# Performance work log

Hardware: AMD Instinct MI355X
Metric: run time of the kernel (lower is better)

Reference implementation:

```python
import jax, jax.numpy as jnp
import numpy as np

DIM = 256
HEAD_DIM = 64
NH = DIM // HEAD_DIM
PS = 2  # fine patch size
EPS = 1e-5


def _conv(x, w, b, stride, pad):
    y = jax.lax.conv_general_dilated(x, w, (stride, stride), ((pad, pad), (pad, pad)),
                                     dimension_numbers=('NCHW', 'OIHW', 'NCHW'))
    return y + b[None, :, None, None]


def _bn(x, g, b, m, v):
    s = g * jax.lax.rsqrt(v + EPS)
    return x * s[None, :, None, None] + (b - m * s)[None, :, None, None]


def setup_inputs() -> dict:
    key = jax.random.key(0)
    ks = jax.random.split(key, 24)
    C = DIM
    d = {}
    d['x'] = jax.random.normal(ks[0], (8, C, 64, 64), jnp.float32)
    # Downsample conv (C->C, k=4, s=2, p=1), torch OIHW layout
    d['w_down'] = jax.random.normal(ks[1], (C, C, 4, 4), jnp.float32) * 0.02
    d['b_down'] = jax.random.normal(ks[2], (C,), jnp.float32) * 0.02
    # coarse to_qkv Linear(64 -> 192), stored as [in, out]
    d['w_qkv_c'] = jax.random.normal(ks[3], (HEAD_DIM, 3 * HEAD_DIM), jnp.float32) * 0.05
    d['b_qkv_c'] = jax.random.normal(ks[4], (3 * HEAD_DIM,), jnp.float32) * 0.02
    # Upsample ConvTranspose2d (torch [in, out, kH, kW] layout)
    d['w_up'] = jax.random.normal(ks[5], (C, C, 4, 4), jnp.float32) * 0.02
    d['b_up'] = jax.random.normal(ks[6], (C,), jnp.float32) * 0.02
    # fine to_qkv Linear(64 -> 192)
    d['w_qkv_f'] = jax.random.normal(ks[7], (HEAD_DIM, 3 * HEAD_DIM), jnp.float32) * 0.05
    d['b_qkv_f'] = jax.random.normal(ks[8], (3 * HEAD_DIM,), jnp.float32) * 0.02
    # DWConv: depthwise 3x3 (groups=C) -> BN -> relu6 -> pointwise 1x1 -> BN -> relu6
    d['w_dw'] = jax.random.normal(ks[9], (C, 1, 3, 3), jnp.float32) * 0.1
    d['bn_dw_g'] = jax.random.uniform(ks[10], (C,), jnp.float32) * 0.5 + 0.75
    d['bn_dw_b'] = jax.random.normal(ks[11], (C,), jnp.float32) * 0.1
    d['bn_dw_m'] = jax.random.normal(ks[12], (C,), jnp.float32) * 0.1
    d['bn_dw_v'] = jax.random.uniform(ks[13], (C,), jnp.float32) + 0.5
    d['w_pw'] = jax.random.normal(ks[14], (C, C, 1, 1), jnp.float32) * 0.05
    d['bn_pw_g'] = jax.random.uniform(ks[15], (C,), jnp.float32) * 0.5 + 0.75
    d['bn_pw_b'] = jax.random.normal(ks[16], (C,), jnp.float32) * 0.1
    d['bn_pw_m'] = jax.random.normal(ks[17], (C,), jnp.float32) * 0.1
    d['bn_pw_v'] = jax.random.uniform(ks[18], (C,), jnp.float32) + 0.5
    return d


def reference(x, w_down, b_down, w_qkv_c, b_qkv_c, w_up, b_up, w_qkv_f, b_qkv_f,
              w_dw, bn_dw_g, bn_dw_b, bn_dw_m, bn_dw_v,
              w_pw, bn_pw_g, bn_pw_b, bn_pw_m, bn_pw_v):
    B, C, H, W = x.shape
    nh, hd = C // HEAD_DIM, HEAD_DIM
    scale = hd ** -0.5

    # ---- CoarseSelfAttention ----
    xd = _conv(x, w_down, b_down, 2, 1)           # [B,C,h,w]
    h, w = xd.shape[2], xd.shape[3]
    P = h * w
    tok = xd.reshape(B, nh, hd, P).transpose(0, 1, 3, 2)   # [B,nh,P,hd]
    q, k, v = jnp.split(tok @ w_qkv_c + b_qkv_c, 3, axis=-1)
    attn = jax.nn.softmax(jnp.einsum('bhqd,bhkd->bhqk', q, k) * scale, axis=-1)
    coarse_score = attn.sum(axis=-2)               # [B,nh,P]
    kf = max(1, P // 4)
    top_k = jax.lax.top_k(coarse_score, kf)[1]     # [B,nh,kf]
    out = jnp.einsum('bhqk,bhkd->bhqd', attn, v)
    out = out.transpose(0, 1, 3, 2).reshape(B, C, h, w)
    # ConvTranspose2d(k=4,s=2,p=1) as lhs-dilated conv with flipped/transposed kernel
    wt = jnp.flip(w_up, (2, 3)).transpose(1, 0, 2, 3)
    coarse = jax.lax.conv_general_dilated(out, wt, (1, 1), ((2, 2), (2, 2)),
                                          lhs_dilation=(2, 2),
                                          dimension_numbers=('NCHW', 'OIHW', 'NCHW'))
    coarse = coarse + b_up[None, :, None, None]
    # F.interpolate to (H,W) is identity here: upsample exactly restores HxW

    # ---- TopkSelfAttention ----
    ph, pw = H // PS, W // PS                      # ph*pw == P
    xh = coarse.reshape(B, nh, hd, ph, PS, pw, PS)
    patches = xh.transpose(0, 1, 2, 3, 5, 4, 6).reshape(B, nh, hd, ph * pw, PS, PS)
    idx = jnp.broadcast_to(top_k[:, :, None, :, None, None], (B, nh, hd, kf, PS, PS))
    sel = jnp.take_along_axis(patches, idx, axis=3)        # [B,nh,hd,kf,PS,PS]
    tokf = sel.reshape(B, nh, hd, kf, PS * PS).transpose(0, 1, 3, 4, 2)
    tokf = tokf.reshape(B, nh, kf * PS * PS, hd)
    qf, kk, vf = jnp.split(tokf @ w_qkv_f + b_qkv_f, 3, axis=-1)
    attnf = jax.nn.softmax(jnp.einsum('bhqd,bhkd->bhqk', qf, kk) * scale, axis=-1)
    outf = jnp.einsum('bhqk,bhkd->bhqd', attnf, vf)
    outf = outf.reshape(B, nh, kf, PS * PS, hd).transpose(0, 1, 2, 4, 3)
    outf = outf.reshape(B, nh, kf, hd, PS, PS)     # [B,nh,kf,hd,PS,PS]
    # scatter selected patches back into zeros (topk indices are unique per b,h)
    res = jnp.zeros((B, nh, ph * pw, hd, PS, PS), x.dtype)
    bi = jnp.arange(B)[:, None, None]
    hi = jnp.arange(nh)[None, :, None]
    res = res.at[bi, hi, top_k].set(outf)
    res = res.transpose(0, 1, 3, 2, 4, 5).reshape(B, nh, hd, ph, pw, PS, PS)
    region = res.transpose(0, 1, 2, 3, 5, 4, 6).reshape(B, C, H, W)

    y = coarse + region

    # ---- DWConv feed-forward ----
    yd = jax.lax.conv_general_dilated(y, w_dw, (1, 1), ((1, 1), (1, 1)),
                                      feature_group_count=C,
                                      dimension_numbers=('NCHW', 'OIHW', 'NCHW'))
    yd = jnp.clip(_bn(yd, bn_dw_g, bn_dw_b, bn_dw_m, bn_dw_v), 0.0, 6.0)
    yp = jax.lax.conv_general_dilated(yd, w_pw, (1, 1), ((0, 0), (0, 0)),
                                      dimension_numbers=('NCHW', 'OIHW', 'NCHW'))
    yp = jnp.clip(_bn(yp, bn_pw_g, bn_pw_b, bn_pw_m, bn_pw_v), 0.0, 6.0)
    return yp
```

## Files before the change

kernel.cpp:

```cpp
#include <hip/hip_runtime.h>
#include <cstdint>
#include <cstddef>


#define EPS_ 1e-5f

typedef short bf16x8_t __attribute__((ext_vector_type(8)));
typedef float f32x4_t __attribute__((ext_vector_type(4)));
#define MFMA16(a, b, c) __builtin_amdgcn_mfma_f32_16x16x32_bf16(a, b, c, 0, 0, 0)

__device__ __forceinline__ void cvt1(float f, unsigned short& h, unsigned short& l) {
  unsigned u = __float_as_uint(f);
  unsigned r = u + 0x7FFFu + ((u >> 16) & 1u);
  h = (unsigned short)(r >> 16);
  float lo = f - __uint_as_float(r & 0xFFFF0000u);
  l = (unsigned short)(__float_as_uint(lo) >> 16);
}
__device__ __forceinline__ unsigned cvtpack(float f) {
  unsigned short h, l;
  cvt1(f, h, l);
  return (unsigned)h | ((unsigned)l << 16);
}
__device__ __forceinline__ void cvt2(float f0, float f1, unsigned& hpack, unsigned& lpack) {
  unsigned u0 = __float_as_uint(f0), u1 = __float_as_uint(f1);
  unsigned r0 = u0 + 0x7FFFu + ((u0 >> 16) & 1u);
  unsigned r1 = u1 + 0x7FFFu + ((u1 >> 16) & 1u);
  hpack = (r0 >> 16) | (r1 & 0xFFFF0000u);
  float l0 = f0 - __uint_as_float(r0 & 0xFFFF0000u);
  float l1 = f1 - __uint_as_float(r1 & 0xFFFF0000u);
  lpack = (__float_as_uint(l0) >> 16) | (__float_as_uint(l1) & 0xFFFF0000u);
}
__device__ __forceinline__ unsigned pk_h(unsigned a, unsigned b) {
  return (a & 0xFFFFu) | (b << 16);
}
__device__ __forceinline__ unsigned pk_l(unsigned a, unsigned b) {
  return (a >> 16) | (b & 0xFFFF0000u);
}

__global__ __launch_bounds__(256) void k_pad_x(
    const float* __restrict__ x, unsigned* __restrict__ xphl) {
  const int plane = blockIdx.x;
  const float* src = x + (size_t)plane * 4096;
  unsigned* dst = xphl + (size_t)plane * 4488;
  for (int e = threadIdx.x; e < 4356; e += 256) {
    int r = e / 66, cc = e - r * 66;
    float v = 0.f;
    if (r >= 1 && r <= 64 && cc >= 1 && cc <= 64) v = src[(r - 1) * 64 + (cc - 1)];
    dst[r * 68 + cc] = cvtpack(v);
  }
}

__global__ __launch_bounds__(256) void k_cvt_wdown(
    const float* __restrict__ w, unsigned short* __restrict__ wh,
    unsigned short* __restrict__ wl) {
  int e = blockIdx.x * 256 + threadIdx.x;
  cvt1(w[e], wh[e], wl[e]);
}

__global__ __launch_bounds__(256) void k_cvt_wqkv(
    const float* __restrict__ wq, unsigned short* __restrict__ wh,
    unsigned short* __restrict__ wl) {
  int e = blockIdx.x * 256 + threadIdx.x;
  int col = e >> 6, d = e & 63;
  float f = wq[d * 192 + col];
  if (col < 64) f *= 0.125f;
  cvt1(f, wh[e], wl[e]);
}

__global__ __launch_bounds__(256) void k_cvt_wup(
    const float* __restrict__ w_up, unsigned short* __restrict__ wth,
    unsigned short* __restrict__ wtl) {
  int e = blockIdx.x * 256 + threadIdx.x;
  int kp = e & 1023, oc = (e >> 10) & 255, c = e >> 18;
  int tap = kp >> 8, ic = kp & 255;
  int tk = tap >> 1, txi = tap & 1;
  int ry = c >> 1, rx = c & 1;
  int ky = (1 - ry) + 2 * tk, kx = (1 - rx) + 2 * txi;
  cvt1(w_up[((size_t)(ic * 256 + oc) * 4 + ky) * 4 + kx], wth[e], wtl[e]);
}

__global__ __launch_bounds__(256) void k_cvt_wpw(
    const float* __restrict__ w, unsigned short* __restrict__ wh,
    unsigned short* __restrict__ wl) {
  int e = blockIdx.x * 256 + threadIdx.x;
  cvt1(w[e], wh[e], wl[e]);
}

__device__ __forceinline__ void mfma_chunk(
    const unsigned short (*Ah)[72], const unsigned short (*Al)[72],
    const unsigned short (*Bh)[72], const unsigned short (*Bl)[72],
    f32x4_t (&acc)[4], int wm, int lane) {
  const int l16 = lane & 15, quad = lane >> 4;
#pragma unroll
  for (int ks = 0; ks < 2; ++ks) {
    int ko = ks * 32 + quad * 8;
    bf16x8_t ah = *(const bf16x8_t*)&Ah[wm + l16][ko];
    bf16x8_t al = *(const bf16x8_t*)&Al[wm + l16][ko];
#pragma unroll
    for (int nt = 0; nt < 4; ++nt) {
      bf16x8_t bh = *(const bf16x8_t*)&Bh[nt * 16 + l16][ko];
      bf16x8_t bl = *(const bf16x8_t*)&Bl[nt * 16 + l16][ko];
      acc[nt] = MFMA16(ah, bh, acc[nt]);
      acc[nt] = MFMA16(ah, bl, acc[nt]);
      acc[nt] = MFMA16(al, bh, acc[nt]);
    }
  }
}

__device__ __forceinline__ void mfma_tile2x2(
    const unsigned short (*Ah)[72], const unsigned short (*Al)[72],
    const unsigned short (*Bh)[72], const unsigned short (*Bl)[72],
    f32x4_t (&acc)[2][2], int wm, int wn, int lane) {
  const int l16 = lane & 15, quad = lane >> 4;
#pragma unroll
  for (int ks = 0; ks < 2; ++ks) {
    int ko = ks * 32 + quad * 8;
    bf16x8_t ah[2], al[2];
#pragma unroll
    for (int mt = 0; mt < 2; ++mt) {
      ah[mt] = *(const bf16x8_t*)&Ah[wm + mt * 16 + l16][ko];
      al[mt] = *(const bf16x8_t*)&Al[wm + mt * 16 + l16][ko];
    }
#pragma unroll
    for (int nt = 0; nt < 2; ++nt) {
      bf16x8_t bh = *(const bf16x8_t*)&Bh[wn + nt * 16 + l16][ko];
      bf16x8_t bl = *(const bf16x8_t*)&Bl[wn + nt * 16 + l16][ko];
#pragma unroll
      for (int mt = 0; mt < 2; ++mt) {
        acc[mt][nt] = MFMA16(ah[mt], bh, acc[mt][nt]);
        acc[mt][nt] = MFMA16(ah[mt], bl, acc[mt][nt]);
        acc[mt][nt] = MFMA16(al[mt], bh, acc[mt][nt]);
      }
    }
  }
}

__device__ __forceinline__ void mfma_tile2x4(
    const unsigned short (*Ah)[72], const unsigned short (*Al)[72],
    const unsigned short (*Bh)[72], const unsigned short (*Bl)[72],
    f32x4_t (&acc)[2][4], int wm, int wn, int lane) {
  const int l16 = lane & 15, quad = lane >> 4;
#pragma unroll
  for (int ks = 0; ks < 2; ++ks) {
    int ko = ks * 32 + quad * 8;
    bf16x8_t ah[2], al[2];
#pragma unroll
    for (int mt = 0; mt < 2; ++mt) {
      ah[mt] = *(const bf16x8_t*)&Ah[wm + mt * 16 + l16][ko];
      al[mt] = *(const bf16x8_t*)&Al[wm + mt * 16 + l16][ko];
    }
#pragma unroll
    for (int nt = 0; nt < 4; ++nt) {
      bf16x8_t bh = *(const bf16x8_t*)&Bh[wn + nt * 16 + l16][ko];
      bf16x8_t bl = *(const bf16x8_t*)&Bl[wn + nt * 16 + l16][ko];
#pragma unroll
      for (int mt = 0; mt < 2; ++mt) {
        acc[mt][nt] = MFMA16(ah[mt], bh, acc[mt][nt]);
        acc[mt][nt] = MFMA16(ah[mt], bl, acc[mt][nt]);
        acc[mt][nt] = MFMA16(al[mt], bh, acc[mt][nt]);
      }
    }
  }
}

__global__ __launch_bounds__(256) void k_conv_down_mfma(
    const unsigned* __restrict__ xphl, const unsigned short* __restrict__ wdh,
    const unsigned short* __restrict__ wdl, const float* __restrict__ bias,
    unsigned* __restrict__ xdhl) {
  __shared__ unsigned short Ah[64][72], Al[64][72], Bh[64][72], Bl[64][72];
  const int t = threadIdx.x;
  const int pix0 = blockIdx.x * 64, oc0 = blockIdx.y * 64;
  const int bimg = pix0 >> 10, pos = pix0 & 1023;
  const int pl = t & 63, icg = t >> 6;
  const int rem = (pix0 + pl) & 1023;
  const int oy = rem >> 5, ox = rem & 31;
  const unsigned* xb = xphl + ((size_t)bimg * 256 + icg) * 4488 + (oy * 2) * 68 + ox * 2;
  const int wave = t >> 6, lane = t & 63, l16 = lane & 15, quad = lane >> 4;
  const int wm = (wave & 1) * 32, wn = (wave >> 1) * 32;
  const int ar = t >> 2, ac = (t & 3) * 16;
  const unsigned short* wra = wdh + (size_t)(oc0 + ar) * 4096 + ac;
  const unsigned short* wrl = wdl + (size_t)(oc0 + ar) * 4096 + ac;
  f32x4_t acc[2][2] = {};
  for (int kb = 0; kb < 4096; kb += 64) {
    bf16x8_t a0 = *(const bf16x8_t*)(wra + kb);
    bf16x8_t a1 = *(const bf16x8_t*)(wra + kb + 8);
    bf16x8_t a2 = *(const bf16x8_t*)(wrl + kb);
    bf16x8_t a3 = *(const bf16x8_t*)(wrl + kb + 8);
    unsigned u[16];
#pragma unroll
    for (int r = 0; r < 4; ++r) {
      uint2 u01 = *(const uint2*)(xb + r * 68);
      uint2 u23 = *(const uint2*)(xb + r * 68 + 2);
      u[4 * r + 0] = u01.x; u[4 * r + 1] = u01.y;
      u[4 * r + 2] = u23.x; u[4 * r + 3] = u23.y;
    }
    unsigned hp[8], lp[8];
#pragma unroll
    for (int j = 0; j < 8; ++j) {
      hp[j] = pk_h(u[2 * j], u[2 * j + 1]);
      lp[j] = pk_l(u[2 * j], u[2 * j + 1]);
    }
    __syncthreads();
    *(bf16x8_t*)&Ah[ar][ac] = a0;
    *(bf16x8_t*)&Ah[ar][ac + 8] = a1;
    *(bf16x8_t*)&Al[ar][ac] = a2;
    *(bf16x8_t*)&Al[ar][ac + 8] = a3;
    *(uint4*)&Bh[pl][icg * 16] = make_uint4(hp[0], hp[1], hp[2], hp[3]);
    *(uint4*)&Bh[pl][icg * 16 + 8] = make_uint4(hp[4], hp[5], hp[6], hp[7]);
    *(uint4*)&Bl[pl][icg * 16] = make_uint4(lp[0], lp[1], lp[2], lp[3]);
    *(uint4*)&Bl[pl][icg * 16 + 8] = make_uint4(lp[4], lp[5], lp[6], lp[7]);
    __syncthreads();
    mfma_tile2x2(Ah, Al, Bh, Bl, acc, wm, wn, lane);
    xb += 4 * 4488;
  }
#pragma unroll
  for (int mt = 0; mt < 2; ++mt)
#pragma unroll
    for (int r = 0; r < 4; ++r) {
      int oc = oc0 + wm + mt * 16 + quad * 4 + r;
      float bv = bias[oc];
#pragma unroll
      for (int nt = 0; nt < 2; ++nt)
        xdhl[((size_t)(bimg * 256 + oc)) * 1024 + pos + wn + nt * 16 + l16] =
            cvtpack(acc[mt][nt][r] + bv);
    }
}

template <int MODE>
__global__ __launch_bounds__(256) void k_qkv_mfma(
    const unsigned* __restrict__ srcp, const float* __restrict__ srcf,
    const unsigned short* __restrict__ wh, const unsigned short* __restrict__ wl,
    const float* __restrict__ bq, const int* __restrict__ topk,
    unsigned short* __restrict__ qh, unsigned short* __restrict__ ql,
    unsigned short* __restrict__ kh, unsigned short* __restrict__ kl,
    unsigned short* __restrict__ vth, unsigned short* __restrict__ vtl) {
  __shared__ unsigned short Ah[64][72], Al[64][72];
  const int t = threadIdx.x;
  const int tok0 = blockIdx.x * 64;
  const int pair = blockIdx.y;
  const int b = pair >> 2, h = pair & 3;
  const int tokl = t & 63, dg = t >> 6;
  unsigned hp[8], lp[8];
  if (MODE == 0) {
    const unsigned* base = srcp + ((size_t)(b * 256 + h * 64 + dg * 16)) * 1024 + tok0 + tokl;
    unsigned u[16];
#pragma unroll
    for (int j = 0; j < 16; ++j) u[j] = base[(size_t)j * 1024];
#pragma unroll
    for (int j = 0; j < 8; ++j) {
      hp[j] = pk_h(u[2 * j], u[2 * j + 1]);
      lp[j] = pk_l(u[2 * j], u[2 * j + 1]);
    }
  } else {
    int tok = tok0 + tokl;
    int pp = topk[pair * 256 + (tok >> 2)];
    int py = (tok >> 1) & 1, px = tok & 1;
    int ry = (pp >> 5) * 2 + py, rx = (pp & 31) * 2 + px;
    const float* base = srcf + ((size_t)(b * 256 + h * 64 + dg * 16)) * 4096 + ry * 64 + rx;
    float fv[16];
#pragma unroll
    for (int j = 0; j < 16; ++j) fv[j] = base[(size_t)j * 4096];
#pragma unroll
    for (int j = 0; j < 8; ++j) cvt2(fv[2 * j], fv[2 * j + 1], hp[j], lp[j]);
  }
  *(uint4*)&Ah[tokl][dg * 16] = make_uint4(hp[0], hp[1], hp[2], hp[3]);
  *(uint4*)&Ah[tokl][dg * 16 + 8] = make_uint4(hp[4], hp[5], hp[6], hp[7]);
  *(uint4*)&Al[tokl][dg * 16] = make_uint4(lp[0], lp[1], lp[2], lp[3]);
  *(uint4*)&Al[tokl][dg * 16 + 8] = make_uint4(lp[4], lp[5], lp[6], lp[7]);
  __syncthreads();
  const int wave = t >> 6, lane = t & 63, l16 = lane & 15, quad = lane >> 4;
  f32x4_t acc[4][3] = {};
#pragma unroll
  for (int ks = 0; ks < 2; ++ks) {
    int ko = ks * 32 + quad * 8;
    bf16x8_t bh0[3], bl0[3];
#pragma unroll
    for (int nt = 0; nt < 3; ++nt) {
      int col = wave * 48 + nt * 16 + l16;
      bh0[nt] = *(const bf16x8_t*)(wh + col * 64 + ko);
      bl0[nt] = *(const bf16x8_t*)(wl + col * 64 + ko);
    }
#pragma unroll
    for (int mt = 0; mt < 4; ++mt) {
      bf16x8_t ah = *(const bf16x8_t*)&Ah[mt * 16 + l16][ko];
      bf16x8_t al = *(const bf16x8_t*)&Al[mt * 16 + l16][ko];
#pragma unroll
      for (int nt = 0; nt < 3; ++nt) {
        acc[mt][nt] = MFMA16(ah, bh0[nt], acc[mt][nt]);
        acc[mt][nt] = MFMA16(ah, bl0[nt], acc[mt][nt]);
        acc[mt][nt] = MFMA16(al, bh0[nt], acc[mt][nt]);
      }
    }
  }
#pragma unroll
  for (int nt = 0; nt < 3; ++nt) {
    int col = wave * 48 + nt * 16 + l16;
    float bqv = bq[col];
    if (col < 64) bqv *= 0.125f;
#pragma unroll
    for (int mt = 0; mt < 4; ++mt) {
#pragma unroll
      for (int r = 0; r < 4; ++r) {
        int tok = tok0 + mt * 16 + quad * 4 + r;
        float val = acc[mt][nt][r] + bqv;
        unsigned short hh, ll;
        cvt1(val, hh, ll);
        if (col < 64) {
          size_t o = ((size_t)pair * 1024 + tok) * 64 + col;
          qh[o] = hh; ql[o] = ll;
        } else if (col < 128) {
          size_t o = ((size_t)pair * 1024 + tok) * 64 + (col - 64);
          kh[o] = hh; kl[o] = ll;
        } else {
          size_t o = ((size_t)pair * 64 + (col - 128)) * 1024 + tok;
          vth[o] = hh; vtl[o] = ll;
        }
      }
    }
  }
}

__global__ __launch_bounds__(256) void k_attn_coarse(
    const unsigned short* __restrict__ qh, const unsigned short* __restrict__ ql,
    const unsigned short* __restrict__ kh, const unsigned short* __restrict__ kl,
    const unsigned short* __restrict__ vth, const unsigned short* __restrict__ vtl,
    float* __restrict__ score, unsigned* __restrict__ outc) {
  __shared__ __align__(16) unsigned short Qb[2][64][72];
  __shared__ __align__(16) unsigned short Kb[2][64][72];
  __shared__ __align__(16) unsigned short Vb[2][64][72];
  __shared__ __align__(16) unsigned short Pb[2][64][72];
  __shared__ float mlW[4][2][64];
  __shared__ float mC[64], lC[64];
  __shared__ float colsum[1024];
  const int t = threadIdx.x;
  const int q0 = blockIdx.x * 64;
  const int pair = blockIdx.y;
  const int wave = t >> 6, lane = t & 63;
  const int l16 = lane & 15, quad = lane >> 4;
  const int wm = wave * 16;
  const int sr = t >> 3, skc = (t & 7) * 8;

  const size_t qbase = ((size_t)pair * 1024 + q0) * 64;
#pragma unroll
  for (int i = 0; i < 2; ++i) {
    int r = sr + i * 32;
    *(bf16x8_t*)&Qb[0][r][skc] = *(const bf16x8_t*)(qh + qbase + (size_t)r * 64 + skc);
    *(bf16x8_t*)&Qb[1][r][skc] = *(const bf16x8_t*)(ql + qbase + (size_t)r * 64 + skc);
  }
#pragma unroll
  for (int i = 0; i < 4; ++i) colsum[t + i * 256] = 0.f;

  const size_t kmbase = (size_t)pair * 1024 * 64;
  const size_t vbase = (size_t)pair * 64 * 1024;

  float mrun[4] = {-1e30f, -1e30f, -1e30f, -1e30f};
  float lrun[4] = {0.f, 0.f, 0.f, 0.f};
  for (int kb = 0; kb < 1024; kb += 64) {
    __syncthreads();
#pragma unroll
    for (int i = 0; i < 2; ++i) {
      int r = sr + i * 32;
      *(bf16x8_t*)&Kb[0][r][skc] = *(const bf16x8_t*)(kh + kmbase + (size_t)(kb + r) * 64 + skc);
      *(bf16x8_t*)&Kb[1][r][skc] = *(const bf16x8_t*)(kl + kmbase + (size_t)(kb + r) * 64 + skc);
    }
    __syncthreads();
    f32x4_t acc[4] = {};
    mfma_chunk(Kb[0], Kb[1], Qb[0], Qb[1], acc, wm, lane);
#pragma unroll
    for (int nt = 0; nt < 4; ++nt) {
      float m0 = fmaxf(fmaxf(acc[nt][0], acc[nt][1]), fmaxf(acc[nt][2], acc[nt][3]));
      m0 = fmaxf(m0, __shfl_xor(m0, 16));
      m0 = fmaxf(m0, __shfl_xor(m0, 32));
      float mn = fmaxf(mrun[nt], m0);
      float s0 = __expf(acc[nt][0] - mn) + __expf(acc[nt][1] - mn) +
                 __expf(acc[nt][2] - mn) + __expf(acc[nt][3] - mn);
      s0 += __shfl_xor(s0, 16);
      s0 += __shfl_xor(s0, 32);
      lrun[nt] = lrun[nt] * __expf(mrun[nt] - mn) + s0;
      mrun[nt] = mn;
    }
  }
  __syncthreads();
  if (quad == 0) {
#pragma unroll
    for (int nt = 0; nt < 4; ++nt) {
      mlW[wave][0][nt * 16 + l16] = mrun[nt];
      mlW[wave][1][nt * 16 + l16] = lrun[nt];
    }
  }
  __syncthreads();
  if (t < 64) {
    float m0 = mlW[0][0][t], m1 = mlW[1][0][t], m2 = mlW[2][0][t], m3 = mlW[3][0][t];
    float mm = fmaxf(fmaxf(m0, m1), fmaxf(m2, m3));
    float ll = mlW[0][1][t] * __expf(m0 - mm) + mlW[1][1][t] * __expf(m1 - mm) +
               mlW[2][1][t] * __expf(m2 - mm) + mlW[3][1][t] * __expf(m3 - mm);
    mC[t] = mm;
    lC[t] = 1.0f / ll;
  }
  __syncthreads();
  float mq[4], il[4];
#pragma unroll
  for (int nt = 0; nt < 4; ++nt) {
    mq[nt] = mC[nt * 16 + l16];
    il[nt] = lC[nt * 16 + l16];
  }

  f32x4_t accO[4] = {};
  for (int kb = 0; kb < 1024; kb += 64) {
    __syncthreads();
#pragma unroll
    for (int i = 0; i < 2; ++i) {
      int r = sr + i * 32;
      *(bf16x8_t*)&Kb[0][r][skc] = *(const bf16x8_t*)(kh + kmbase + (size_t)(kb + r) * 64 + skc);
      *(bf16x8_t*)&Kb[1][r][skc] = *(const bf16x8_t*)(kl + kmbase + (size_t)(kb + r) * 64 + skc);
      *(bf16x8_t*)&Vb[0][r][skc] = *(const bf16x8_t*)(vth + vbase + (size_t)r * 1024 + kb + skc);
      *(bf16x8_t*)&Vb[1][r][skc] = *(const bf16x8_t*)(vtl + vbase + (size_t)r * 1024 + kb + skc);
    }
    __syncthreads();
    f32x4_t acc[4] = {};
    mfma_chunk(Kb[0], Kb[1], Qb[0], Qb[1], acc, wm, lane);
    float P[4][4];
#pragma unroll
    for (int nt = 0; nt < 4; ++nt)
#pragma unroll
      for (int r = 0; r < 4; ++r) P[nt][r] = __expf(acc[nt][r] - mq[nt]) * il[nt];
#pragma unroll
    for (int r = 0; r < 4; ++r) {
      float cs = P[0][r] + P[1][r] + P[2][r] + P[3][r];
      cs += __shfl_xor(cs, 1);
      cs += __shfl_xor(cs, 2);
      cs += __shfl_xor(cs, 4);
      cs += __shfl_xor(cs, 8);
      if (l16 == 0) colsum[kb + wm + quad * 4 + r] += cs;
    }
#pragma unroll
    for (int nt = 0; nt < 4; ++nt) {
      unsigned h01, l01, h23, l23;
      cvt2(P[nt][0], P[nt][1], h01, l01);
      cvt2(P[nt][2], P[nt][3], h23, l23);
      *(uint2*)&Pb[0][nt * 16 + l16][wm + quad * 4] = make_uint2(h01, h23);
      *(uint2*)&Pb[1][nt * 16 + l16][wm + quad * 4] = make_uint2(l01, l23);
    }
    __syncthreads();
    mfma_chunk(Pb[0], Pb[1], Vb[0], Vb[1], accO, wm, lane);
  }
  __syncthreads();

#pragma unroll
  for (int i = 0; i < 4; ++i)
    atomicAdd(&score[pair * 1024 + t + i * 256], colsum[t + i * 256]);
  float (*Tr)[68] = reinterpret_cast<float(*)[68]>(&Pb[0][0][0]);
#pragma unroll
  for (int nt = 0; nt < 4; ++nt)
#pragma unroll
    for (int r = 0; r < 4; ++r)
      Tr[nt * 16 + l16][wm + quad * 4 + r] = accO[nt][r];
  __syncthreads();
  const int b = pair >> 2, h = pair & 3;
#pragma unroll
  for (int i = 0; i < 16; ++i) {
    int e = t + i * 256;
    int d = e >> 6, ql_ = e & 63;
    int pix = q0 + ql_;
    int iy = (pix >> 5) + 1, ix = (pix & 31) + 1;
    outc[((size_t)(b * 256 + h * 64 + d)) * 1156 + iy * 34 + ix] = cvtpack(Tr[d][ql_]);
  }
}

__global__ __launch_bounds__(256) void k_attn_fine(
    const unsigned short* __restrict__ qh, const unsigned short* __restrict__ ql,
    const unsigned short* __restrict__ kh, const unsigned short* __restrict__ kl,
    const unsigned short* __restrict__ vth, const unsigned short* __restrict__ vtl,
    float* __restrict__ outf) {
  __shared__ __align__(16) unsigned short Qb[2][64][72];
  __shared__ __align__(16) unsigned short Kb[2][64][72];
  __shared__ __align__(16) unsigned short Vb[2][64][72];
  __shared__ __align__(16) unsigned short Pb[2][64][72];
  __shared__ float m_run[64], l_run[64], alphaS[64];
  __shared__ float mWc[4][64], sWc[4][64];
  const int t = threadIdx.x;
  const int q0 = blockIdx.x * 64;
  const int pair = blockIdx.y;
  const int wave = t >> 6, lane = t & 63;
  const int l16 = lane & 15, quad = lane >> 4;
  const int wm = wave * 16;
  const int sr = t >> 3, skc = (t & 7) * 8;

  const size_t qbase = ((size_t)pair * 1024 + q0) * 64;
#pragma unroll
  for (int i = 0; i < 2; ++i) {
    int r = sr + i * 32;
    *(bf16x8_t*)&Qb[0][r][skc] = *(const bf16x8_t*)(qh + qbase + (size_t)r * 64 + skc);
    *(bf16x8_t*)&Qb[1][r][skc] = *(const bf16x8_t*)(ql + qbase + (size_t)r * 64 + skc);
  }
  if (t < 64) { m_run[t] = -1e30f; l_run[t] = 0.f; }

  const size_t kmbase = (size_t)pair * 1024 * 64;
  const size_t vbase = (size_t)pair * 64 * 1024;

  f32x4_t accO[4] = {};
  for (int kb = 0; kb < 1024; kb += 64) {
    __syncthreads();
#pragma unroll
    for (int i = 0; i < 2; ++i) {
      int r = sr + i * 32;
      *(bf16x8_t*)&Kb[0][r][skc] = *(const bf16x8_t*)(kh + kmbase + (size_t)(kb + r) * 64 + skc);
      *(bf16x8_t*)&Kb[1][r][skc] = *(const bf16x8_t*)(kl + kmbase + (size_t)(kb + r) * 64 + skc);
      *(bf16x8_t*)&Vb[0][r][skc] = *(const bf16x8_t*)(vth + vbase + (size_t)r * 1024 + kb + skc);
      *(bf16x8_t*)&Vb[1][r][skc] = *(const bf16x8_t*)(vtl + vbase + (size_t)r * 1024 + kb + skc);
    }
    __syncthreads();
    f32x4_t acc[4] = {};
    mfma_chunk(Kb[0], Kb[1], Qb[0], Qb[1], acc, wm, lane);
#pragma unroll
    for (int nt = 0; nt < 4; ++nt) {
      float m0 = fmaxf(fmaxf(acc[nt][0], acc[nt][1]), fmaxf(acc[nt][2], acc[nt][3]));
      m0 = fmaxf(m0, __shfl_xor(m0, 16));
      m0 = fmaxf(m0, __shfl_xor(m0, 32));
      if (quad == 0) mWc[wave][nt * 16 + l16] = m0;
    }
    __syncthreads();
    if (t < 64) {
      float mn = fmaxf(fmaxf(fmaxf(mWc[0][t], mWc[1][t]), fmaxf(mWc[2][t], mWc[3][t])),
                       m_run[t]);
      alphaS[t] = __expf(m_run[t] - mn);
      m_run[t] = mn;
    }
    __syncthreads();
    float P[4][4];
#pragma unroll
    for (int nt = 0; nt < 4; ++nt) {
      float mn = m_run[nt * 16 + l16];
#pragma unroll
      for (int r = 0; r < 4; ++r) P[nt][r] = __expf(acc[nt][r] - mn);
      float s0 = P[nt][0] + P[nt][1] + P[nt][2] + P[nt][3];
      s0 += __shfl_xor(s0, 16);
      s0 += __shfl_xor(s0, 32);
      if (quad == 0) sWc[wave][nt * 16 + l16] = s0;
      unsigned h01, l01, h23, l23;
      cvt2(P[nt][0], P[nt][1], h01, l01);
      cvt2(P[nt][2], P[nt][3], h23, l23);
      *(uint2*)&Pb[0][nt * 16 + l16][wm + quad * 4] = make_uint2(h01, h23);
      *(uint2*)&Pb[1][nt * 16 + l16][wm + quad * 4] = make_uint2(l01, l23);
    }
#pragma unroll
    for (int r = 0; r < 4; ++r) {
      float a = alphaS[wm + quad * 4 + r];
#pragma unroll
      for (int nt = 0; nt < 4; ++nt) accO[nt][r] *= a;
    }
    __syncthreads();
    if (t < 64)
      l_run[t] = l_run[t] * alphaS[t] + (sWc[0][t] + sWc[1][t] + sWc[2][t] + sWc[3][t]);
    mfma_chunk(Pb[0], Pb[1], Vb[0], Vb[1], accO, wm, lane);
  }
  __syncthreads();
#pragma unroll
  for (int r = 0; r < 4; ++r) {
    float invl = 1.0f / l_run[wm + quad * 4 + r];
    int qm = q0 + wm + quad * 4 + r;
#pragma unroll
    for (int nt = 0; nt < 4; ++nt)
      outf[((size_t)pair * 1024 + qm) * 64 + nt * 16 + l16] = accO[nt][r] * invl;
  }
}

__global__ __launch_bounds__(256) void k_topk(
    const float* __restrict__ score, int* __restrict__ idx) {
  __shared__ unsigned long long key[1024];
  const int pair = blockIdx.x;
  const int t = threadIdx.x;
#pragma unroll
  for (int j = 0; j < 4; ++j) {
    int i = t + j * 256;
    unsigned u = __float_as_uint(score[pair * 1024 + i]);
    u = u ^ ((u & 0x80000000u) ? 0xFFFFFFFFu : 0x80000000u);
    u = ~u;
    key[i] = ((unsigned long long)u << 32) | (unsigned)i;
  }
  __syncthreads();
  for (int k = 2; k <= 1024; k <<= 1) {
    for (int j = k >> 1; j > 0; j >>= 1) {
      for (int w = 0; w < 4; ++w) {
        int i = t + w * 256;
        int l = i ^ j;
        if (l > i) {
          bool up = ((i & k) == 0);
          unsigned long long a = key[i], b = key[l];
          if ((a > b) == up) { key[i] = b; key[l] = a; }
        }
      }
      __syncthreads();
    }
  }
  idx[pair * 256 + t] = (int)(key[t] & 0xFFFFFFFFu);
}

__global__ __launch_bounds__(256) void k_convT_mfma(
    const unsigned* __restrict__ inp, const unsigned short* __restrict__ wth,
    const unsigned short* __restrict__ wtl, const float* __restrict__ bias,
    float* __restrict__ out) {
  __shared__ unsigned short Ah[64][72], Al[64][72];
  __shared__ unsigned short Bh[128][72], Bl[128][72];
  const int t = threadIdx.x;
  const int pix0 = blockIdx.x * 128;
  const int oc0 = blockIdx.y * 64;
  const int cls = blockIdx.z;
  const int ry = cls >> 1, rx = cls & 1;
  const int b = pix0 >> 10;
  const int wave = t >> 6, lane = t & 63;
  const int l16 = lane & 15, quad = lane >> 4;
  const int wm = (wave & 1) * 32, wn = (wave >> 1) * 64;
  const int pl = t & 127, icg = t >> 7;
  const int remg = (pix0 + pl) & 1023;
  const int tyy = remg >> 5, txx = remg & 31;
  const int ar = t >> 2, ac = (t & 3) * 16;
  const size_t wbase = ((size_t)cls * 256 + oc0 + ar) * 1024 + ac;
  f32x4_t acc[2][4] = {};
  for (int kb = 0; kb < 1024; kb += 64) {
    const int tap = kb >> 8, ic0 = kb & 255;
    const int tk = tap >> 1, txi = tap & 1;
    const int iy = tyy + ry + 1 - tk, ix = txx + rx + 1 - txi;
    const unsigned* p = inp + (size_t)(b * 256 + ic0 + icg * 32) * 1156 + iy * 34 + ix;
    unsigned u[32];
#pragma unroll
    for (int j = 0; j < 32; ++j) u[j] = p[(size_t)j * 1156];
    unsigned hp[16], lpk[16];
#pragma unroll
    for (int j = 0; j < 16; ++j) {
      hp[j] = pk_h(u[2 * j], u[2 * j + 1]);
      lpk[j] = pk_l(u[2 * j], u[2 * j + 1]);
    }
    bf16x8_t a0 = *(const bf16x8_t*)(wth + wbase + kb);
    bf16x8_t a1 = *(const bf16x8_t*)(wth + wbase + kb + 8);
    bf16x8_t a2 = *(const bf16x8_t*)(wtl + wbase + kb);
    bf16x8_t a3 = *(const bf16x8_t*)(wtl + wbase + kb + 8);
    __syncthreads();
    *(bf16x8_t*)&Ah[ar][ac] = a0;
    *(bf16x8_t*)&Ah[ar][ac + 8] = a1;
    *(bf16x8_t*)&Al[ar][ac] = a2;
    *(bf16x8_t*)&Al[ar][ac + 8] = a3;
    {
      int kc = icg * 32;
      *(uint4*)&Bh[pl][kc] = make_uint4(hp[0], hp[1], hp[2], hp[3]);
      *(uint4*)&Bh[pl][kc + 8] = make_uint4(hp[4], hp[5], hp[6], hp[7]);
      *(uint4*)&Bh[pl][kc + 16] = make_uint4(hp[8], hp[9], hp[10], hp[11]);
      *(uint4*)&Bh[pl][kc + 24] = make_uint4(hp[12], hp[13], hp[14], hp[15]);
      *(uint4*)&Bl[pl][kc] = make_uint4(lpk[0], lpk[1], lpk[2], lpk[3]);
      *(uint4*)&Bl[pl][kc + 8] = make_uint4(lpk[4], lpk[5], lpk[6], lpk[7]);
      *(uint4*)&Bl[pl][kc + 16] = make_uint4(lpk[8], lpk[9], lpk[10], lpk[11]);
      *(uint4*)&Bl[pl][kc + 24] = make_uint4(lpk[12], lpk[13], lpk[14], lpk[15]);
    }
    __syncthreads();
    mfma_tile2x4(Ah, Al, Bh, Bl, acc, wm, wn, lane);
  }
#pragma unroll
  for (int mt = 0; mt < 2; ++mt)
#pragma unroll
    for (int r = 0; r < 4; ++r) {
      int oc = oc0 + wm + mt * 16 + quad * 4 + r;
      float bvs = bias[oc];
#pragma unroll
      for (int nt = 0; nt < 4; ++nt) {
        int pix = pix0 + wn + nt * 16 + l16;
        int rem2 = pix & 1023;
        int y = (rem2 >> 5) * 2 + ry, xx = (rem2 & 31) * 2 + rx;
        out[((size_t)(b * 256 + oc) * 64 + y) * 64 + xx] = acc[mt][nt][r] + bvs;
      }
    }
}

__global__ __launch_bounds__(256) void k_scatter(
    const float* __restrict__ outf, const int* __restrict__ idx,
    float* __restrict__ y) {
  int g = blockIdx.x * 256 + threadIdx.x;
  int pair = g >> 16;
  int rem = g & 65535;
  int tok = rem >> 6, d = rem & 63;
  int b = pair >> 2, h = pair & 3;
  int pp = idx[pair * 256 + (tok >> 2)];
  int py = (tok >> 1) & 1, px = tok & 1;
  int ry = (pp >> 5) * 2 + py, rx = (pp & 31) * 2 + px;
  y[((size_t)(b * 256 + h * 64 + d) * 64 + ry) * 64 + rx] += outf[g];
}

__global__ __launch_bounds__(256) void k_dwconv(
    const float* __restrict__ y, const float* __restrict__ wdw,
    const float* __restrict__ g, const float* __restrict__ bb,
    const float* __restrict__ m, const float* __restrict__ vv,
    unsigned* __restrict__ ydhl) {
  int gi = blockIdx.x * 256 + threadIdx.x;
  int x = gi & 63, yy = (gi >> 6) & 63, ch = (gi >> 12) & 255, b = gi >> 20;
  const float* plane = y + (size_t)(b * 256 + ch) * 4096;
  const float* wc = wdw + ch * 9;
  float s = 0.f;
#pragma unroll
  for (int ky = 0; ky < 3; ++ky) {
    int iy = yy + ky - 1;
    if (iy < 0 || iy >= 64) continue;
#pragma unroll
    for (int kx = 0; kx < 3; ++kx) {
      int ix = x + kx - 1;
      if (ix < 0 || ix >= 64) continue;
      s = fmaf(plane[iy * 64 + ix], wc[ky * 3 + kx], s);
    }
  }
  float sc = g[ch] * rsqrtf(vv[ch] + EPS_);
  float val = s * sc + (bb[ch] - m[ch] * sc);
  ydhl[gi] = cvtpack(fminf(fmaxf(val, 0.f), 6.f));
}

__global__ __launch_bounds__(256) void k_pw_mfma(
    const unsigned* __restrict__ ydhl, const unsigned short* __restrict__ wh,
    const unsigned short* __restrict__ wl, const float* __restrict__ g,
    const float* __restrict__ bb, const float* __restrict__ m,
    const float* __restrict__ vv, float* __restrict__ out) {
  __shared__ unsigned short Ah[64][72], Al[64][72];
  __shared__ unsigned short Bh[128][72], Bl[128][72];
  const int t = threadIdx.x;
  const int pix0 = blockIdx.x * 128;
  const int oc0 = blockIdx.y * 64;
  const int b = pix0 >> 12, pos0 = pix0 & 4095;
  const int wave = t >> 6, lane = t & 63;
  const int l16 = lane & 15, quad = lane >> 4;
  const int wm = (wave & 1) * 32, wn = (wave >> 1) * 64;
  const int pl = t & 127, icg = t >> 7;
  const int ar = t >> 2, ac = (t & 3) * 16;
  f32x4_t acc[2][4] = {};
  for (int kb = 0; kb < 256; kb += 64) {
    const unsigned* p = ydhl + (size_t)(b * 256 + kb + icg * 32) * 4096 + pos0 + pl;
    unsigned u[32];
#pragma unroll
    for (int j = 0; j < 32; ++j) u[j] = p[(size_t)j * 4096];
    unsigned hp[16], lpk[16];
#pragma unroll
    for (int j = 0; j < 16; ++j) {
      hp[j] = pk_h(u[2 * j], u[2 * j + 1]);
      lpk[j] = pk_l(u[2 * j], u[2 * j + 1]);
    }
    bf16x8_t a0 = *(const bf16x8_t*)(wh + (size_t)(oc0 + ar) * 256 + kb + ac);
    bf16x8_t a1 = *(const bf16x8_t*)(wh + (size_t)(oc0 + ar) * 256 + kb + ac + 8);
    bf16x8_t a2 = *(const bf16x8_t*)(wl + (size_t)(oc0 + ar) * 256 + kb + ac);
    bf16x8_t a3 = *(const bf16x8_t*)(wl + (size_t)(oc0 + ar) * 256 + kb + ac + 8);
    __syncthreads();
    *(bf16x8_t*)&Ah[ar][ac] = a0;
    *(bf16x8_t*)&Ah[ar][ac + 8] = a1;
    *(bf16x8_t*)&Al[ar][ac] = a2;
    *(bf16x8_t*)&Al[ar][ac + 8] = a3;
    {
      int kc = icg * 32;
      *(uint4*)&Bh[pl][kc] = make_uint4(hp[0], hp[1], hp[2], hp[3]);
      *(uint4*)&Bh[pl][kc + 8] = make_uint4(hp[4], hp[5], hp[6], hp[7]);
      *(uint4*)&Bh[pl][kc + 16] = make_uint4(hp[8], hp[9], hp[10], hp[11]);
      *(uint4*)&Bh[pl][kc + 24] = make_uint4(hp[12], hp[13], hp[14], hp[15]);
      *(uint4*)&Bl[pl][kc] = make_uint4(lpk[0], lpk[1], lpk[2], lpk[3]);
      *(uint4*)&Bl[pl][kc + 8] = make_uint4(lpk[4], lpk[5], lpk[6], lpk[7]);
      *(uint4*)&Bl[pl][kc + 16] = make_uint4(lpk[8], lpk[9], lpk[10], lpk[11]);
      *(uint4*)&Bl[pl][kc + 24] = make_uint4(lpk[12], lpk[13], lpk[14], lpk[15]);
    }
    __syncthreads();
    mfma_tile2x4(Ah, Al, Bh, Bl, acc, wm, wn, lane);
  }
#pragma unroll
  for (int mt = 0; mt < 2; ++mt)
#pragma unroll
    for (int r = 0; r < 4; ++r) {
      int oc = oc0 + wm + mt * 16 + quad * 4 + r;
      float sc = g[oc] * rsqrtf(vv[oc] + EPS_);
      float off = bb[oc] - m[oc] * sc;
#pragma unroll
      for (int nt = 0; nt < 4; ++nt) {
        int pix = pos0 + wn + nt * 16 + l16;
        float val = fminf(fmaxf(acc[mt][nt][r] * sc + off, 0.f), 6.f);
        out[(size_t)(b * 256 + oc) * 4096 + pix] = val;
      }
    }
}

extern "C" void kernel_launch(void* const* d_in, const int* in_sizes, int n_in,
                              void* d_out, int out_size, void* d_ws, size_t ws_size,
                              hipStream_t stream) {
  (void)in_sizes; (void)n_in; (void)out_size; (void)ws_size;
  const float* x       = (const float*)d_in[0];
  const float* w_down  = (const float*)d_in[1];
  const float* b_down  = (const float*)d_in[2];
  const float* w_qkv_c = (const float*)d_in[3];
  const float* b_qkv_c = (const float*)d_in[4];
  const float* w_up    = (const float*)d_in[5];
  const float* b_up    = (const float*)d_in[6];
  const float* w_qkv_f = (const float*)d_in[7];
  const float* b_qkv_f = (const float*)d_in[8];
  const float* w_dw    = (const float*)d_in[9];
  const float* bn_dw_g = (const float*)d_in[10];
  const float* bn_dw_b = (const float*)d_in[11];
  const float* bn_dw_m = (const float*)d_in[12];
  const float* bn_dw_v = (const float*)d_in[13];
  const float* w_pw    = (const float*)d_in[14];
  const float* bn_pw_g = (const float*)d_in[15];
  const float* bn_pw_b = (const float*)d_in[16];
  const float* bn_pw_m = (const float*)d_in[17];
  const float* bn_pw_v = (const float*)d_in[18];

  float* ws = (float*)d_ws;
  unsigned*       xphl   = (unsigned*)ws;
  unsigned*       ydhl   = (unsigned*)ws;
  unsigned short* qh     = (unsigned short*)(ws + 33554432);
  unsigned short* ql     = (unsigned short*)(ws + 34603008);
  unsigned short* kh     = (unsigned short*)(ws + 35651584);
  unsigned short* kl     = (unsigned short*)(ws + 36700160);
  unsigned short* vth    = (unsigned short*)(ws + 37748736);
  unsigned short* vtl    = (unsigned short*)(ws + 38797312);
  unsigned*       xdhl   = (unsigned*)(ws + 39845888);
  unsigned*       outcphl= (unsigned*)(ws + 41943040);
  float*          coarse = ws + 44310528;
  float*          outf   = ws + 52699136;
  float*          score  = ws + 54796288;
  unsigned short* wdh    = (unsigned short*)(ws + 54829056);
  unsigned short* wdl    = (unsigned short*)(ws + 55353344);
  unsigned short* wt_hi  = (unsigned short*)(ws + 55877632);
  unsigned short* wt_lo  = (unsigned short*)(ws + 56401920);
  unsigned short* wpw_hi = (unsigned short*)(ws + 56926208);
  unsigned short* wpw_lo = (unsigned short*)(ws + 56958976);
  unsigned short* wqh_c  = (unsigned short*)(ws + 56991744);
  unsigned short* wql_c  = (unsigned short*)(ws + 56997888);
  unsigned short* wqh_f  = (unsigned short*)(ws + 57004032);
  unsigned short* wql_f  = (unsigned short*)(ws + 57010176);
  int*            idx    = (int*)(ws + 57016320);

  hipMemsetAsync(score, 0, 32768 * sizeof(float), stream);
  hipMemsetAsync(outcphl, 0, (size_t)2367488 * sizeof(unsigned), stream);
  k_pad_x<<<2048, 256, 0, stream>>>(x, xphl);
  k_cvt_wdown<<<4096, 256, 0, stream>>>(w_down, wdh, wdl);
  k_cvt_wqkv<<<48, 256, 0, stream>>>(w_qkv_c, wqh_c, wql_c);
  k_cvt_wqkv<<<48, 256, 0, stream>>>(w_qkv_f, wqh_f, wql_f);
  k_cvt_wup<<<4096, 256, 0, stream>>>(w_up, wt_hi, wt_lo);
  k_cvt_wpw<<<256, 256, 0, stream>>>(w_pw, wpw_hi, wpw_lo);

  k_conv_down_mfma<<<dim3(128, 4), 256, 0, stream>>>(xphl, wdh, wdl, b_down, xdhl);
  k_qkv_mfma<0><<<dim3(16, 32), 256, 0, stream>>>(xdhl, nullptr, wqh_c, wql_c, b_qkv_c,
                                                  nullptr, qh, ql, kh, kl, vth, vtl);
  k_attn_coarse<<<dim3(16, 32), 256, 0, stream>>>(qh, ql, kh, kl, vth, vtl, score, outcphl);
  k_topk<<<32, 256, 0, stream>>>(score, idx);
  k_convT_mfma<<<dim3(64, 4, 4), 256, 0, stream>>>(outcphl, wt_hi, wt_lo, b_up, coarse);

  k_qkv_mfma<1><<<dim3(16, 32), 256, 0, stream>>>(nullptr, coarse, wqh_f, wql_f, b_qkv_f,
                                                  idx, qh, ql, kh, kl, vth, vtl);
  k_attn_fine<<<dim3(16, 32), 256, 0, stream>>>(qh, ql, kh, kl, vth, vtl, outf);
  k_scatter<<<8192, 256, 0, stream>>>(outf, idx, coarse);
  k_dwconv<<<32768, 256, 0, stream>>>(coarse, w_dw, bn_dw_g, bn_dw_b, bn_dw_m, bn_dw_v, ydhl);
  k_pw_mfma<<<dim3(256, 4), 256, 0, stream>>>(ydhl, wpw_hi, wpw_lo, bn_pw_g, bn_pw_b,
                                              bn_pw_m, bn_pw_v, (float*)d_out);
}
```

Before: 604.9 us.

## Register-prefetch next K-chunk global loads across MFMA GEMM and attention loops

Each MFMA tiled loop (downsample conv, both attention passes, the second attention kernel, transposed conv, pointwise conv) now issues the global loads for the next K-chunk into registers before the MFMA work on the current chunk. The current chunk is still staged through shared memory. This is meant to hide global memory latency behind the matrix math, at the cost of more live registers per thread, which may reduce occupancy.

```diff
diff --git a/kernel.cpp b/kernel.cpp
--- a/kernel.cpp
+++ b/kernel.cpp
@@ -181,24 +181,25 @@
   const unsigned short* wra = wdh + (size_t)(oc0 + ar) * 4096 + ac;
   const unsigned short* wrl = wdl + (size_t)(oc0 + ar) * 4096 + ac;
   f32x4_t acc[2][2] = {};
+  bf16x8_t a0, a1, a2, a3;
+  uint2 u01[4], u23[4];
+  a0 = *(const bf16x8_t*)(wra);
+  a1 = *(const bf16x8_t*)(wra + 8);
+  a2 = *(const bf16x8_t*)(wrl);
+  a3 = *(const bf16x8_t*)(wrl + 8);
+#pragma unroll
+  for (int r = 0; r < 4; ++r) {
+    u01[r] = *(const uint2*)(xb + r * 68);
+    u23[r] = *(const uint2*)(xb + r * 68 + 2);
+  }
   for (int kb = 0; kb < 4096; kb += 64) {
-    bf16x8_t a0 = *(const bf16x8_t*)(wra + kb);
-    bf16x8_t a1 = *(const bf16x8_t*)(wra + kb + 8);
-    bf16x8_t a2 = *(const bf16x8_t*)(wrl + kb);
-    bf16x8_t a3 = *(const bf16x8_t*)(wrl + kb + 8);
-    unsigned u[16];
+    unsigned hp[8], lp[8];
 #pragma unroll
     for (int r = 0; r < 4; ++r) {
-      uint2 u01 = *(const uint2*)(xb + r * 68);
-      uint2 u23 = *(const uint2*)(xb + r * 68 + 2);
-      u[4 * r + 0] = u01.x; u[4 * r + 1] = u01.y;
-      u[4 * r + 2] = u23.x; u[4 * r + 3] = u23.y;
-    }
-    unsigned hp[8], lp[8];
-#pragma unroll
-    for (int j = 0; j < 8; ++j) {
-      hp[j] = pk_h(u[2 * j], u[2 * j + 1]);
-      lp[j] = pk_l(u[2 * j], u[2 * j + 1]);
+      hp[2 * r]     = pk_h(u01[r].x, u01[r].y);
+      lp[2 * r]     = pk_l(u01[r].x, u01[r].y);
+      hp[2 * r + 1] = pk_h(u23[r].x, u23[r].y);
+      lp[2 * r + 1] = pk_l(u23[r].x, u23[r].y);
     }
     __syncthreads();
     *(bf16x8_t*)&Ah[ar][ac] = a0;
@@ -209,9 +210,20 @@
     *(uint4*)&Bh[pl][icg * 16 + 8] = make_uint4(hp[4], hp[5], hp[6], hp[7]);
     *(uint4*)&Bl[pl][icg * 16] = make_uint4(lp[0], lp[1], lp[2], lp[3]);
     *(uint4*)&Bl[pl][icg * 16 + 8] = make_uint4(lp[4], lp[5], lp[6], lp[7]);
+    if (kb + 64 < 4096) {
+      xb += 4 * 4488;
+      a0 = *(const bf16x8_t*)(wra + kb + 64);
+      a1 = *(const bf16x8_t*)(wra + kb + 64 + 8);
+      a2 = *(const bf16x8_t*)(wrl + kb + 64);
+      a3 = *(const bf16x8_t*)(wrl + kb + 64 + 8);
+#pragma unroll
+      for (int r = 0; r < 4; ++r) {
+        u01[r] = *(const uint2*)(xb + r * 68);
+        u23[r] = *(const uint2*)(xb + r * 68 + 2);
+      }
+    }
     __syncthreads();
     mfma_tile2x2(Ah, Al, Bh, Bl, acc, wm, wn, lane);
-    xb += 4 * 4488;
   }
 #pragma unroll
   for (int mt = 0; mt < 2; ++mt)
@@ -353,6 +365,14 @@
   const size_t kmbase = (size_t)pair * 1024 * 64;
   const size_t vbase = (size_t)pair * 64 * 1024;
 
+  bf16x8_t pk0[2], pk1[2];
+#pragma unroll
+  for (int i = 0; i < 2; ++i) {
+    int r = sr + i * 32;
+    pk0[i] = *(const bf16x8_t*)(kh + kmbase + (size_t)r * 64 + skc);
+    pk1[i] = *(const bf16x8_t*)(kl + kmbase + (size_t)r * 64 + skc);
+  }
+
   float mrun[4] = {-1e30f, -1e30f, -1e30f, -1e30f};
   float lrun[4] = {0.f, 0.f, 0.f, 0.f};
   for (int kb = 0; kb < 1024; kb += 64) {
@@ -360,8 +380,16 @@
 #pragma unroll
     for (int i = 0; i < 2; ++i) {
       int r = sr + i * 32;
-      *(bf16x8_t*)&Kb[0][r][skc] = *(const bf16x8_t*)(kh + kmbase + (size_t)(kb + r) * 64 + skc);
-      *(bf16x8_t*)&Kb[1][r][skc] = *(const bf16x8_t*)(kl + kmbase + (size_t)(kb + r) * 64 + skc);
+      *(bf16x8_t*)&Kb[0][r][skc] = pk0[i];
+      *(bf16x8_t*)&Kb[1][r][skc] = pk1[i];
+    }
+    if (kb + 64 < 1024) {
+#pragma unroll
+      for (int i = 0; i < 2; ++i) {
+        int r = sr + i * 32;
+        pk0[i] = *(const bf16x8_t*)(kh + kmbase + (size_t)(kb + 64 + r) * 64 + skc);
+        pk1[i] = *(const bf16x8_t*)(kl + kmbase + (size_t)(kb + 64 + r) * 64 + skc);
+      }
     }
     __syncthreads();
     f32x4_t acc[4] = {};
@@ -380,6 +408,15 @@
       mrun[nt] = mn;
     }
   }
+  bf16x8_t pv0[2], pv1[2];
+#pragma unroll
+  for (int i = 0; i < 2; ++i) {
+    int r = sr + i * 32;
+    pk0[i] = *(const bf16x8_t*)(kh + kmbase + (size_t)r * 64 + skc);
+    pk1[i] = *(const bf16x8_t*)(kl + kmbase + (size_t)r * 64 + skc);
+    pv0[i] = *(const bf16x8_t*)(vth + vbase + (size_t)r * 1024 + skc);
+    pv1[i] = *(const bf16x8_t*)(vtl + vbase + (size_t)r * 1024 + skc);
+  }
   __syncthreads();
   if (quad == 0) {
 #pragma unroll
@@ -411,10 +448,20 @@
 #pragma unroll
     for (int i = 0; i < 2; ++i) {
       int r = sr + i * 32;
-      *(bf16x8_t*)&Kb[0][r][skc] = *(const bf16x8_t*)(kh + kmbase + (size_t)(kb + r) * 64 + skc);
-      *(bf16x8_t*)&Kb[1][r][skc] = *(const bf16x8_t*)(kl + kmbase + (size_t)(kb + r) * 64 + skc);
-      *(bf16x8_t*)&Vb[0][r][skc] = *(const bf16x8_t*)(vth + vbase + (size_t)r * 1024 + kb + skc);
-      *(bf16x8_t*)&Vb[1][r][skc] = *(const bf16x8_t*)(vtl + vbase + (size_t)r * 1024 + kb + skc);
+      *(bf16x8_t*)&Kb[0][r][skc] = pk0[i];
+      *(bf16x8_t*)&Kb[1][r][skc] = pk1[i];
+      *(bf16x8_t*)&Vb[0][r][skc] = pv0[i];
+      *(bf16x8_t*)&Vb[1][r][skc] = pv1[i];
+    }
+    if (kb + 64 < 1024) {
+#pragma unroll
+      for (int i = 0; i < 2; ++i) {
+        int r = sr + i * 32;
+        pk0[i] = *(const bf16x8_t*)(kh + kmbase + (size_t)(kb + 64 + r) * 64 + skc);
+        pk1[i] = *(const bf16x8_t*)(kl + kmbase + (size_t)(kb + 64 + r) * 64 + skc);
+        pv0[i] = *(const bf16x8_t*)(vth + vbase + (size_t)r * 1024 + kb + 64 + skc);
+        pv1[i] = *(const bf16x8_t*)(vtl + vbase + (size_t)r * 1024 + kb + 64 + skc);
+      }
     }
     __syncthreads();
     f32x4_t acc[4] = {};
@@ -498,16 +545,36 @@
   const size_t kmbase = (size_t)pair * 1024 * 64;
   const size_t vbase = (size_t)pair * 64 * 1024;
 
+  bf16x8_t pk0[2], pk1[2], pv0[2], pv1[2];
+#pragma unroll
+  for (int i = 0; i < 2; ++i) {
+    int r = sr + i * 32;
+    pk0[i] = *(const bf16x8_t*)(kh + kmbase + (size_t)r * 64 + skc);
+    pk1[i] = *(const bf16x8_t*)(kl + kmbase + (size_t)r * 64 + skc);
+    pv0[i] = *(const bf16x8_t*)(vth + vbase + (size_t)r * 1024 + skc);
+    pv1[i] = *(const bf16x8_t*)(vtl + vbase + (size_t)r * 1024 + skc);
+  }
+
   f32x4_t accO[4] = {};
   for (int kb = 0; kb < 1024; kb += 64) {
     __syncthreads();
 #pragma unroll
     for (int i = 0; i < 2; ++i) {
       int r = sr + i * 32;
-      *(bf16x8_t*)&Kb[0][r][skc] = *(const bf16x8_t*)(kh + kmbase + (size_t)(kb + r) * 64 + skc);
-      *(bf16x8_t*)&Kb[1][r][skc] = *(const bf16x8_t*)(kl + kmbase + (size_t)(kb + r) * 64 + skc);
-      *(bf16x8_t*)&Vb[0][r][skc] = *(const bf16x8_t*)(vth + vbase + (size_t)r * 1024 + kb + skc);
-      *(bf16x8_t*)&Vb[1][r][skc] = *(const bf16x8_t*)(vtl + vbase + (size_t)r * 1024 + kb + skc);
+      *(bf16x8_t*)&Kb[0][r][skc] = pk0[i];
+      *(bf16x8_t*)&Kb[1][r][skc] = pk1[i];
+      *(bf16x8_t*)&Vb[0][r][skc] = pv0[i];
+      *(bf16x8_t*)&Vb[1][r][skc] = pv1[i];
+    }
+    if (kb + 64 < 1024) {
+#pragma unroll
+      for (int i = 0; i < 2; ++i) {
+        int r = sr + i * 32;
+        pk0[i] = *(const bf16x8_t*)(kh + kmbase + (size_t)(kb + 64 + r) * 64 + skc);
+        pk1[i] = *(const bf16x8_t*)(kl + kmbase + (size_t)(kb + 64 + r) * 64 + skc);
+        pv0[i] = *(const bf16x8_t*)(vth + vbase + (size_t)r * 1024 + kb + 64 + skc);
+        pv1[i] = *(const bf16x8_t*)(vtl + vbase + (size_t)r * 1024 + kb + 64 + skc);
+      }
     }
     __syncthreads();
     f32x4_t acc[4] = {};
@@ -617,24 +684,25 @@
   const int ar = t >> 2, ac = (t & 3) * 16;
   const size_t wbase = ((size_t)cls * 256 + oc0 + ar) * 1024 + ac;
   f32x4_t acc[2][4] = {};
+  bf16x8_t a0, a1, a2, a3;
+  unsigned u[32];
+  {
+    const int iy = tyy + ry + 1, ix = txx + rx + 1;
+    const unsigned* p = inp + (size_t)(b * 256 + icg * 32) * 1156 + iy * 34 + ix;
+#pragma unroll
+    for (int j = 0; j < 32; ++j) u[j] = p[(size_t)j * 1156];
+    a0 = *(const bf16x8_t*)(wth + wbase);
+    a1 = *(const bf16x8_t*)(wth + wbase + 8);
+    a2 = *(const bf16x8_t*)(wtl + wbase);
+    a3 = *(const bf16x8_t*)(wtl + wbase + 8);
+  }
   for (int kb = 0; kb < 1024; kb += 64) {
-    const int tap = kb >> 8, ic0 = kb & 255;
-    const int tk = tap >> 1, txi = tap & 1;
-    const int iy = tyy + ry + 1 - tk, ix = txx + rx + 1 - txi;
-    const unsigned* p = inp + (size_t)(b * 256 + ic0 + icg * 32) * 1156 + iy * 34 + ix;
-    unsigned u[32];
-#pragma unroll
-    for (int j = 0; j < 32; ++j) u[j] = p[(size_t)j * 1156];
     unsigned hp[16], lpk[16];
 #pragma unroll
     for (int j = 0; j < 16; ++j) {
       hp[j] = pk_h(u[2 * j], u[2 * j + 1]);
       lpk[j] = pk_l(u[2 * j], u[2 * j + 1]);
     }
-    bf16x8_t a0 = *(const bf16x8_t*)(wth + wbase + kb);
-    bf16x8_t a1 = *(const bf16x8_t*)(wth + wbase + kb + 8);
-    bf16x8_t a2 = *(const bf16x8_t*)(wtl + wbase + kb);
-    bf16x8_t a3 = *(const bf16x8_t*)(wtl + wbase + kb + 8);
     __syncthreads();
     *(bf16x8_t*)&Ah[ar][ac] = a0;
     *(bf16x8_t*)&Ah[ar][ac + 8] = a1;
@@ -650,6 +718,19 @@
       *(uint4*)&Bl[pl][kc + 8] = make_uint4(lpk[4], lpk[5], lpk[6], lpk[7]);
       *(uint4*)&Bl[pl][kc + 16] = make_uint4(lpk[8], lpk[9], lpk[10], lpk[11]);
       *(uint4*)&Bl[pl][kc + 24] = make_uint4(lpk[12], lpk[13], lpk[14], lpk[15]);
+    }
+    if (kb + 64 < 1024) {
+      const int kn = kb + 64;
+      const int tap = kn >> 8, ic0 = kn & 255;
+      const int tk = tap >> 1, txi = tap & 1;
+      const int iy = tyy + ry + 1 - tk, ix = txx + rx + 1 - txi;
+      const unsigned* p = inp + (size_t)(b * 256 + ic0 + icg * 32) * 1156 + iy * 34 + ix;
+#pragma unroll
+      for (int j = 0; j < 32; ++j) u[j] = p[(size_t)j * 1156];
+      a0 = *(const bf16x8_t*)(wth + wbase + kn);
+      a1 = *(const bf16x8_t*)(wth + wbase + kn + 8);
+      a2 = *(const bf16x8_t*)(wtl + wbase + kn);
+      a3 = *(const bf16x8_t*)(wtl + wbase + kn + 8);
     }
     __syncthreads();
     mfma_tile2x4(Ah, Al, Bh, Bl, acc, wm, wn, lane);
@@ -727,21 +808,24 @@
   const int pl = t & 127, icg = t >> 7;
   const int ar = t >> 2, ac = (t & 3) * 16;
   f32x4_t acc[2][4] = {};
+  bf16x8_t a0, a1, a2, a3;
+  unsigned u[32];
+  {
+    const unsigned* p = ydhl + (size_t)(b * 256 + icg * 32) * 4096 + pos0 + pl;
+#pragma unroll
+    for (int j = 0; j < 32; ++j) u[j] = p[(size_t)j * 4096];
+    a0 = *(const bf16x8_t*)(wh + (size_t)(oc0 + ar) * 256 + ac);
+    a1 = *(const bf16x8_t*)(wh + (size_t)(oc0 + ar) * 256 + ac + 8);
+    a2 = *(const bf16x8_t*)(wl + (size_t)(oc0 + ar) * 256 + ac);
+    a3 = *(const bf16x8_t*)(wl + (size_t)(oc0 + ar) * 256 + ac + 8);
+  }
   for (int kb = 0; kb < 256; kb += 64) {
-    const unsigned* p = ydhl + (size_t)(b * 256 + kb + icg * 32) * 4096 + pos0 + pl;
-    unsigned u[32];
-#pragma unroll
-    for (int j = 0; j < 32; ++j) u[j] = p[(size_t)j * 4096];
     unsigned hp[16], lpk[16];
 #pragma unroll
     for (int j = 0; j < 16; ++j) {
       hp[j] = pk_h(u[2 * j], u[2 * j + 1]);
       lpk[j] = pk_l(u[2 * j], u[2 * j + 1]);
     }
-    bf16x8_t a0 = *(const bf16x8_t*)(wh + (size_t)(oc0 + ar) * 256 + kb + ac);
-    bf16x8_t a1 = *(const bf16x8_t*)(wh + (size_t)(oc0 + ar) * 256 + kb + ac + 8);
-    bf16x8_t a2 = *(const bf16x8_t*)(wl + (size_t)(oc0 + ar) * 256 + kb + ac);
-    bf16x8_t a3 = *(const bf16x8_t*)(wl + (size_t)(oc0 + ar) * 256 + kb + ac + 8);
     __syncthreads();
     *(bf16x8_t*)&Ah[ar][ac] = a0;
     *(bf16x8_t*)&Ah[ar][ac + 8] = a1;
@@ -757,6 +841,16 @@
       *(uint4*)&Bl[pl][kc + 8] = make_uint4(lpk[4], lpk[5], lpk[6], lpk[7]);
       *(uint4*)&Bl[pl][kc + 16] = make_uint4(lpk[8], lpk[9], lpk[10], lpk[11]);
       *(uint4*)&Bl[pl][kc + 24] = make_uint4(lpk[12], lpk[13], lpk[14], lpk[15]);
+    }
+    if (kb + 64 < 256) {
+      const int kn = kb + 64;
+      const unsigned* p = ydhl + (size_t)(b * 256 + kn + icg * 32) * 4096 + pos0 + pl;
+#pragma unroll
+      for (int j = 0; j < 32; ++j) u[j] = p[(size_t)j * 4096];
+      a0 = *(const bf16x8_t*)(wh + (size_t)(oc0 + ar) * 256 + kn + ac);
+      a1 = *(const bf16x8_t*)(wh + (size_t)(oc0 + ar) * 256 + kn + ac + 8);
+      a2 = *(const bf16x8_t*)(wl + (size_t)(oc0 + ar) * 256 + kn + ac);
+      a3 = *(const bf16x8_t*)(wl + (size_t)(oc0 + ar) * 256 + kn + ac + 8);
     }
     __syncthreads();
     mfma_tile2x4(Ah, Al, Bh, Bl, acc, wm, wn, lane);
```

Result: no change. 610.5 us (+0.9%).
